# Kernel optimization log

Measured on AMD Instinct MI355X. Metric: run time of the kernel, lower is better.

## Reference

```python
import jax, jax.numpy as jnp
import numpy as np

B = 32          # graphs in batch
NP = 1000       # nodes per graph (uniform -> static TopK)
N = B * NP      # total nodes
DEG = 10
E = N * DEG     # intra-graph edges
H, D = 4, 128   # heads, per-head dim (GATConv(32,128,heads=4))
F_IN = 32
HD = H * D      # 512
K = int(np.ceil(0.8 * NP))  # TopKPooling ratio=0.8 -> 800 kept per graph
SLOPE = 0.2     # GATConv leaky_relu negative slope


def setup_inputs() -> dict:
    key = jax.random.key(0)
    ks = jax.random.split(key, 16)
    x = jax.random.normal(ks[0], (N, F_IN), jnp.float32)
    off = (jnp.arange(B, dtype=jnp.int64) * NP)[:, None]
    src = (jax.random.randint(ks[1], (B, NP * DEG), 0, NP) + off).reshape(-1)
    dst = (jax.random.randint(ks[2], (B, NP * DEG), 0, NP) + off).reshape(-1)
    edge_index = jnp.stack([src, dst]).astype(jnp.int64)
    batch = jnp.repeat(jnp.arange(B, dtype=jnp.int64), NP)
    edge_attr = jax.random.normal(ks[3], (E, 16), jnp.float32)
    # GATConv params
    W = jax.random.normal(ks[4], (F_IN, HD), jnp.float32) / np.sqrt(F_IN)
    att_src = jax.random.normal(ks[5], (H, D), jnp.float32) * 0.1
    att_dst = jax.random.normal(ks[6], (H, D), jnp.float32) * 0.1
    bias = jnp.zeros((HD,), jnp.float32)
    # TopKPooling weight
    topk_w = jax.random.normal(ks[7], (HD,), jnp.float32)
    # MLP head
    lin1_w = jax.random.normal(ks[8], (2 * HD, 128), jnp.float32) / np.sqrt(2 * HD)
    lin1_b = jnp.zeros((128,), jnp.float32)
    lin2_w = jax.random.normal(ks[9], (128, 64), jnp.float32) / np.sqrt(128)
    lin2_b = jnp.zeros((64,), jnp.float32)
    lin3_w = jax.random.normal(ks[10], (64, 8), jnp.float32) / np.sqrt(64)
    lin3_b = jnp.zeros((8,), jnp.float32)
    return dict(x=x, edge_index=edge_index, batch=batch, edge_attr=edge_attr,
                W=W, att_src=att_src, att_dst=att_dst, bias=bias, topk_w=topk_w,
                lin1_w=lin1_w, lin1_b=lin1_b, lin2_w=lin2_w, lin2_b=lin2_b,
                lin3_w=lin3_w, lin3_b=lin3_b)


def reference(x, edge_index, batch, edge_attr, W, att_src, att_dst, bias, topk_w,
              lin1_w, lin1_b, lin2_w, lin2_b, lin3_w, lin3_b):
    # ---- GATConv(32,128,heads=4), concat, default self-loops ----
    loop = jnp.arange(N, dtype=edge_index.dtype)
    src = jnp.concatenate([edge_index[0], loop])
    dst = jnp.concatenate([edge_index[1], loop])
    h = (x @ W).reshape(N, H, D)                       # [N,H,D]
    a_s = jnp.einsum('nhd,hd->nh', h, att_src)         # [N,H]
    a_d = jnp.einsum('nhd,hd->nh', h, att_dst)
    e = jax.nn.leaky_relu(a_s[src] + a_d[dst], SLOPE)  # [E2,H]
    m = jax.ops.segment_max(e, dst, num_segments=N)    # per-dst softmax (stable)
    ex = jnp.exp(e - m[dst])
    denom = jax.ops.segment_sum(ex, dst, num_segments=N)
    alpha = ex / denom[dst]                            # [E2,H]
    agg = jax.ops.segment_sum(alpha[:, :, None] * h[src], dst, num_segments=N)
    x1 = jax.nn.relu(agg.reshape(N, HD) + bias)        # [N,512]
    # ---- TopKPooling(512, ratio=0.8), tanh nonlinearity ----
    score = jnp.tanh((x1 @ topk_w) / jnp.linalg.norm(topk_w))  # [N]
    vals, idx = jax.lax.top_k(score.reshape(B, NP), K)         # [B,K]
    xg = x1.reshape(B, NP, HD)
    xs = jnp.take_along_axis(xg, idx[:, :, None], axis=1) * vals[:, :, None]
    # ---- global max + mean pool, MLP head (eval: dropout = identity) ----
    x2 = jnp.concatenate([xs.max(axis=1), xs.mean(axis=1)], axis=-1)  # [B,1024]
    h1 = jax.nn.relu(x2 @ lin1_w + lin1_b)
    h2 = jax.nn.relu(h1 @ lin2_w + lin2_b)
    return jax.nn.log_softmax(h2 @ lin3_w + lin3_b, axis=-1)  # [B,8]
```

## Files before the change

kernel.cpp:

```cpp
#include <hip/hip_runtime.h>
#include <hip/hip_fp16.h>
#include <math.h>


#define N_NODES 32000
#define B_GRAPHS 32
#define NPG 1000
#define DEGC 10
#define E_EDGES (N_NODES*DEGC)
#define HD 512
#define F_IN 32
#define KKEEP 800
#define SLOPE 0.2f
#define CAP 32

__global__ void prep_kernel(const float* __restrict__ W, const float* __restrict__ att_src,
                            const float* __restrict__ att_dst, const float* __restrict__ topk_w,
                            float* __restrict__ Ws, float* __restrict__ Wd, float* __restrict__ misc,
                            int* __restrict__ counts)
{
    int tid = threadIdx.x;
    if (blockIdx.x > 0) {
        int i = (blockIdx.x - 1)*256 + tid;
        if (i < N_NODES/4) ((int4*)counts)[i] = make_int4(0,0,0,0);
        return;
    }
    if (tid < 128) {
        int f = tid >> 2, hh = tid & 3;
        float s1 = 0.f, s2 = 0.f;
        for (int d = 0; d < 128; ++d) {
            float w = W[f*HD + hh*128 + d];
            s1 = fmaf(w, att_src[hh*128 + d], s1);
            s2 = fmaf(w, att_dst[hh*128 + d], s2);
        }
        Ws[f*4+hh] = s1;
        Wd[f*4+hh] = s2;
    }
    __shared__ float red[256];
    float tw0 = topk_w[tid], tw1 = topk_w[tid+256];
    red[tid] = tw0*tw0 + tw1*tw1;
    __syncthreads();
    for (int s = 128; s > 0; s >>= 1) { if (tid < s) red[tid] += red[tid+s]; __syncthreads(); }
    if (tid == 0) misc[0] = 1.0f / sqrtf(red[0]);
}

#define NPB 32
#define CH_BLOCKS 1000
#define BS_BLOCKS 128
__global__ __launch_bounds__(256) void stage1_kernel(
    const float* __restrict__ x, const float* __restrict__ W,
    const float* __restrict__ Ws, const float* __restrict__ Wd,
    const int* __restrict__ dst,
    __half* __restrict__ h, float* __restrict__ a_s, float* __restrict__ a_d,
    int* __restrict__ counts, int* __restrict__ slots)
{
    int b = blockIdx.x;
    int tid = threadIdx.x;
    if (b < CH_BLOCKS) {
        __shared__ float s_x[NPB*F_IN];
        int n0 = (b & 7)*4000 + (b >> 3)*NPB;
        float wc0[F_IN], wc1[F_IN];
        #pragma unroll
        for (int f = 0; f < F_IN; ++f) {
            float2 wp = *(const float2*)(W + f*HD + 2*tid);
            wc0[f] = wp.x;
            wc1[f] = wp.y;
        }
        const float4* xg = (const float4*)(x + (size_t)n0*F_IN);
        float4* sx4 = (float4*)s_x;
        if (tid < NPB*F_IN/4) sx4[tid] = xg[tid];
        __syncthreads();
        for (int n = 0; n < NPB; ++n) {
            const float4* xr = (const float4*)(s_x + n*F_IN);
            float acc0 = 0.f, acc1 = 0.f;
            #pragma unroll
            for (int f4 = 0; f4 < F_IN/4; ++f4) {
                float4 xv = xr[f4];
                acc0 = fmaf(xv.x, wc0[f4*4+0], acc0); acc1 = fmaf(xv.x, wc1[f4*4+0], acc1);
                acc0 = fmaf(xv.y, wc0[f4*4+1], acc0); acc1 = fmaf(xv.y, wc1[f4*4+1], acc1);
                acc0 = fmaf(xv.z, wc0[f4*4+2], acc0); acc1 = fmaf(xv.z, wc1[f4*4+2], acc1);
                acc0 = fmaf(xv.w, wc0[f4*4+3], acc0); acc1 = fmaf(xv.w, wc1[f4*4+3], acc1);
            }
            *(__half2*)(h + (size_t)(n0+n)*HD + 2*tid) = __floats2half2_rn(acc0, acc1);
        }
        {
            int n = tid >> 3, hh = (tid >> 1) & 3, which = tid & 1;
            const float* Wx = which ? Wd : Ws;
            const float* xr = s_x + n*F_IN;
            float s = 0.f;
            #pragma unroll
            for (int f = 0; f < F_IN; ++f) s = fmaf(xr[f], Wx[f*4+hh], s);
            float* dp = which ? a_d : a_s;
            dp[(size_t)(n0+n)*4 + hh] = s;
        }
    } else {
        int i = (b - CH_BLOCKS)*256 + tid;
        int stride = BS_BLOCKS*256;
        for (; i < E_EDGES; i += stride) {
            int d = dst[i];
            int p = atomicAdd(&counts[d], 1);
            if (p < CAP) slots[d*CAP + p] = i;
        }
    }
}

__global__ __launch_bounds__(256) void gat_agg_kernel(
    const __half* __restrict__ h, const float* __restrict__ a_s, const float* __restrict__ a_d,
    const int* __restrict__ counts, const int* __restrict__ slots, const int* __restrict__ esrc,
    const float* __restrict__ bias, const float* __restrict__ topk_w, const float* __restrict__ misc,
    __half* __restrict__ x1, float* __restrict__ scores)
{
    __shared__ int    s_src[4][CAP];
    __shared__ float4 s_al4[4][CAP];
    int tid = threadIdx.x;
    int wid = tid >> 6, lane = tid & 63;
    int grp  = (blockIdx.x & 7) * 1000 + (blockIdx.x >> 3);
    int node = grp*4 + wid;
    int deg  = min(counts[node], CAP);

    int key = (lane < deg) ? slots[node*CAP + lane] : (0x7FFF0000 + lane);
    int rank = 0;
    for (int j = 0; j < deg; ++j) rank += (__shfl(key, j, 64) < key);
    if (lane >= deg) rank = lane;
    int sorted_eid = __builtin_amdgcn_ds_permute(rank << 2, key);

    int src = node;
    if (lane < deg) src = esrc[sorted_eid];

    float4 ad    = *(const float4*)(a_d + (size_t)node*4);
    float4 aself = *(const float4*)(a_s + (size_t)node*4);
    float4 asrc  = make_float4(0.f,0.f,0.f,0.f);
    if (lane < deg) asrc = *(const float4*)(a_s + (size_t)src*4);

    float ex[4], exs[4];
    {
        float u;
        u = asrc.x + ad.x;  ex[0]  = u > 0.f ? u : SLOPE*u;
        u = asrc.y + ad.y;  ex[1]  = u > 0.f ? u : SLOPE*u;
        u = asrc.z + ad.z;  ex[2]  = u > 0.f ? u : SLOPE*u;
        u = asrc.w + ad.w;  ex[3]  = u > 0.f ? u : SLOPE*u;
        u = aself.x + ad.x; exs[0] = __expf(u > 0.f ? u : SLOPE*u);
        u = aself.y + ad.y; exs[1] = __expf(u > 0.f ? u : SLOPE*u);
        u = aself.z + ad.z; exs[2] = __expf(u > 0.f ? u : SLOPE*u);
        u = aself.w + ad.w; exs[3] = __expf(u > 0.f ? u : SLOPE*u);
    }
    float al[4], alself[4];
    #pragma unroll
    for (int hh = 0; hh < 4; ++hh) {
        float e = (lane < deg) ? __expf(ex[hh]) : 0.f;
        float den = e;
        #pragma unroll
        for (int msk = 1; msk < 64; msk <<= 1) den += __shfl_xor(den, msk, 64);
        den += exs[hh];
        float inv = __builtin_amdgcn_rcpf(den);
        al[hh]     = e * inv;
        alself[hh] = exs[hh] * inv;
    }
    if (lane < deg) {
        s_src[wid][lane] = src;
        s_al4[wid][lane] = make_float4(al[0], al[1], al[2], al[3]);
    }
    __syncthreads();

    int head = lane >> 4;
    const __half* hb = h + lane*8;
    const float* alw = (const float*)&s_al4[wid][0];
    float f0=0.f,f1=0.f,f2=0.f,f3=0.f,f4=0.f,f5=0.f,f6=0.f,f7=0.f;
    #define MIX_LO(ACC,A,Q) asm("v_fma_mix_f32 %0, %1, %2, %0 op_sel_hi:[0,1,0]" : "+v"(ACC) : "v"(A), "v"(Q))
    #define MIX_HI(ACC,A,Q) asm("v_fma_mix_f32 %0, %1, %2, %0 op_sel:[0,1,0] op_sel_hi:[0,1,0]" : "+v"(ACC) : "v"(A), "v"(Q))
    #define EDGE_STEP(E_IDX)                                                          \
        {   int se = s_src[wid][E_IDX];                                               \
            float av = alw[(E_IDX)*4 + head];                                         \
            uint4 q = *(const uint4*)(hb + (size_t)se*HD);                            \
            MIX_LO(f0, av, q.x); MIX_HI(f1, av, q.x);                                 \
            MIX_LO(f2, av, q.y); MIX_HI(f3, av, q.y);                                 \
            MIX_LO(f4, av, q.z); MIX_HI(f5, av, q.z);                                 \
            MIX_LO(f6, av, q.w); MIX_HI(f7, av, q.w); }
    int e = 0;
    for (; e + 2 <= deg; e += 2) { EDGE_STEP(e); EDGE_STEP(e+1); }
    if (e < deg) EDGE_STEP(e);
    #undef EDGE_STEP
    {
        float a01 = (head & 1) ? alself[1] : alself[0];
        float a23 = (head & 1) ? alself[3] : alself[2];
        float av  = (head & 2) ? a23 : a01;
        uint4 q = *(const uint4*)(hb + (size_t)node*HD);
        MIX_LO(f0, av, q.x); MIX_HI(f1, av, q.x);
        MIX_LO(f2, av, q.y); MIX_HI(f3, av, q.y);
        MIX_LO(f4, av, q.z); MIX_HI(f5, av, q.z);
        MIX_LO(f6, av, q.w); MIX_HI(f7, av, q.w);
    }
    #undef MIX_LO
    #undef MIX_HI

    int c0 = lane*8;
    float4 b0 = *(const float4*)(bias + c0);
    float4 b1 = *(const float4*)(bias + c0 + 4);
    float v0 = fmaxf(f0 + b0.x, 0.f), v1 = fmaxf(f1 + b0.y, 0.f);
    float v2 = fmaxf(f2 + b0.z, 0.f), v3 = fmaxf(f3 + b0.w, 0.f);
    float v4 = fmaxf(f4 + b1.x, 0.f), v5 = fmaxf(f5 + b1.y, 0.f);
    float v6 = fmaxf(f6 + b1.z, 0.f), v7 = fmaxf(f7 + b1.w, 0.f);
    {
        __half2 p0 = __floats2half2_rn(v0, v1);
        __half2 p1 = __floats2half2_rn(v2, v3);
        __half2 p2 = __floats2half2_rn(v4, v5);
        __half2 p3 = __floats2half2_rn(v6, v7);
        uint4 pk;
        pk.x = *(unsigned*)&p0; pk.y = *(unsigned*)&p1;
        pk.z = *(unsigned*)&p2; pk.w = *(unsigned*)&p3;
        *(uint4*)(x1 + (size_t)node*HD + c0) = pk;
    }

    float4 tw0 = *(const float4*)(topk_w + c0);
    float4 tw1 = *(const float4*)(topk_w + c0 + 4);
    float p = v0*tw0.x + v1*tw0.y + v2*tw0.z + v3*tw0.w
            + v4*tw1.x + v5*tw1.y + v6*tw1.z + v7*tw1.w;
    #pragma unroll
    for (int msk = 1; msk < 64; msk <<= 1) p += __shfl_xor(p, msk, 64);
    if (lane == 0) {
        float dotv = p * misc[0];
        float eu   = __expf(2.f * fabsf(dotv));
        float th   = 1.f - 2.f/(eu + 1.f);
        scores[node] = copysignf(th, dotv);
    }
}

__global__ __launch_bounds__(256) void topk_kernel(const float* __restrict__ scores,
                                                   int* __restrict__ kept_ids,
                                                   float* __restrict__ kept_vals)
{
    int g = blockIdx.x, part = blockIdx.y;
    __shared__ float s[NPG];
    int tid = threadIdx.x;
    for (int i = tid; i < NPG; i += 256) s[i] = scores[g*NPG + i];
    __syncthreads();
    int i = part*250 + tid;
    if (tid < 250) {
        float si = s[i];
        int rank = 0;
        for (int j = 0; j < NPG; ++j) {
            float sj = s[j];
            rank += (sj > si) || (sj == si && j < i);
        }
        if (rank < KKEEP) {
            kept_ids[g*KKEEP + rank]  = g*NPG + i;
            kept_vals[g*KKEEP + rank] = si;
        }
    }
}

#define RCHUNK 50
#define NCHUNK 16
__global__ __launch_bounds__(128) void pool_partial_kernel(
    const __half* __restrict__ x1, const int* __restrict__ kept_ids,
    const float* __restrict__ kept_vals, float* __restrict__ pmax, float* __restrict__ psum)
{
    int bid = blockIdx.x;
    int k = bid & 7, q = bid >> 3;
    int g = k*4 + (q & 3), c = q >> 2;
    int tid = threadIdx.x;
    __shared__ int   ids[RCHUNK];
    __shared__ float vals[RCHUNK];
    if (tid < RCHUNK) {
        ids[tid]  = kept_ids[g*KKEEP + c*RCHUNK + tid];
        vals[tid] = kept_vals[g*KKEEP + c*RCHUNK + tid];
    }
    __syncthreads();
    float4 mxA = make_float4(-INFINITY,-INFINITY,-INFINITY,-INFINITY), mxB = mxA;
    float4 smA = make_float4(0.f,0.f,0.f,0.f), smB = smA;
    for (int r = 0; r < RCHUNK; r += 2) {
        const __half2* pA = (const __half2*)(x1 + (size_t)ids[r]*HD + tid*4);
        const __half2* pB = (const __half2*)(x1 + (size_t)ids[r+1]*HD + tid*4);
        __half2 qA0 = pA[0], qA1 = pA[1], qB0 = pB[0], qB1 = pB[1];
        float2 a0 = __half22float2(qA0), a1 = __half22float2(qA1);
        float2 b0 = __half22float2(qB0), b1 = __half22float2(qB1);
        float lA = vals[r], lB = vals[r+1];
        float4 vA = make_float4(a0.x*lA, a0.y*lA, a1.x*lA, a1.y*lA);
        float4 vB = make_float4(b0.x*lB, b0.y*lB, b1.x*lB, b1.y*lB);
        mxA.x = fmaxf(mxA.x, vA.x); mxA.y = fmaxf(mxA.y, vA.y);
        mxA.z = fmaxf(mxA.z, vA.z); mxA.w = fmaxf(mxA.w, vA.w);
        mxB.x = fmaxf(mxB.x, vB.x); mxB.y = fmaxf(mxB.y, vB.y);
        mxB.z = fmaxf(mxB.z, vB.z); mxB.w = fmaxf(mxB.w, vB.w);
        smA.x += vA.x; smA.y += vA.y; smA.z += vA.z; smA.w += vA.w;
        smB.x += vB.x; smB.y += vB.y; smB.z += vB.z; smB.w += vB.w;
    }
    float4 mx, sm;
    mx.x = fmaxf(mxA.x, mxB.x); mx.y = fmaxf(mxA.y, mxB.y);
    mx.z = fmaxf(mxA.z, mxB.z); mx.w = fmaxf(mxA.w, mxB.w);
    sm.x = smA.x + smB.x; sm.y = smA.y + smB.y;
    sm.z = smA.z + smB.z; sm.w = smA.w + smB.w;
    *(float4*)(pmax + (size_t)(g*NCHUNK + c)*HD + tid*4) = mx;
    *(float4*)(psum + (size_t)(g*NCHUNK + c)*HD + tid*4) = sm;
}

__global__ __launch_bounds__(256) void mlp_kernel(
    const float* __restrict__ pmax, const float* __restrict__ psum,
    const float* __restrict__ w1, const float* __restrict__ b1,
    const float* __restrict__ w2, const float* __restrict__ b2,
    const float* __restrict__ w3, const float* __restrict__ b3,
    float* __restrict__ out)
{
    int g = blockIdx.x;
    int tid = threadIdx.x;
    __shared__ float sx[1024];
    __shared__ float part1[8][128];
    __shared__ float sh1[128];
    __shared__ float part2[4][64];
    __shared__ float sh2[64];
    __shared__ float part3[8][8];
    __shared__ float slog[8];

    {
        int half = tid >> 7;
        int c4 = tid & 127;
        const float* basep = half ? psum : pmax;
        float4 r = *(const float4*)(basep + (size_t)(g*NCHUNK)*HD + c4*4);
        #pragma unroll
        for (int c = 1; c < NCHUNK; ++c) {
            float4 v = *(const float4*)(basep + (size_t)(g*NCHUNK + c)*HD + c4*4);
            if (half) { r.x += v.x; r.y += v.y; r.z += v.z; r.w += v.w; }
            else {
                r.x = fmaxf(r.x, v.x); r.y = fmaxf(r.y, v.y);
                r.z = fmaxf(r.z, v.z); r.w = fmaxf(r.w, v.w);
            }
        }
        if (half) { const float inv = 1.0f/KKEEP; r.x *= inv; r.y *= inv; r.z *= inv; r.w *= inv; }
        *(float4*)(sx + half*512 + c4*4) = r;
    }
    __syncthreads();

    {
        int ks = tid >> 5, tc = tid & 31;
        const float* w1p = w1 + (size_t)(ks*128)*128 + tc*4;
        const float* sxp = sx + ks*128;
        float4 acc = make_float4(0.f,0.f,0.f,0.f);
        #pragma unroll 8
        for (int k = 0; k < 128; ++k) {
            float xk = sxp[k];
            float4 w = *(const float4*)(w1p + (size_t)k*128);
            acc.x = fmaf(xk, w.x, acc.x); acc.y = fmaf(xk, w.y, acc.y);
            acc.z = fmaf(xk, w.z, acc.z); acc.w = fmaf(xk, w.w, acc.w);
        }
        *(float4*)(&part1[ks][tc*4]) = acc;
    }
    __syncthreads();
    if (tid < 128) {
        float s = b1[tid];
        #pragma unroll
        for (int p = 0; p < 8; ++p) s += part1[p][tid];
        sh1[tid] = fmaxf(s, 0.0f);
    }
    __syncthreads();

    {
        int ks2 = tid >> 6, to = tid & 63;
        float a = 0.f;
        #pragma unroll 8
        for (int k = 0; k < 32; ++k) {
            int kk = ks2*32 + k;
            a = fmaf(sh1[kk], w2[kk*64 + to], a);
        }
        part2[ks2][to] = a;
    }
    __syncthreads();
    if (tid < 64) {
        float s = b2[tid];
        #pragma unroll
        for (int p = 0; p < 4; ++p) s += part2[p][tid];
        sh2[tid] = fmaxf(s, 0.0f);
    }
    __syncthreads();

    if (tid < 64) {
        int ks3 = tid >> 3, o = tid & 7;
        float a = 0.f;
        #pragma unroll
        for (int k = 0; k < 8; ++k) {
            int kk = ks3*8 + k;
            a = fmaf(sh2[kk], w3[kk*8 + o], a);
        }
        part3[ks3][o] = a;
    }
    __syncthreads();
    if (tid < 8) {
        float s = b3[tid];
        #pragma unroll
        for (int p = 0; p < 8; ++p) s += part3[p][tid];
        slog[tid] = s;
    }
    __syncthreads();
    if (tid == 0) {
        float m = slog[0];
        for (int i = 1; i < 8; ++i) m = fmaxf(m, slog[i]);
        float ssum = 0.0f;
        for (int i = 0; i < 8; ++i) ssum += expf(slog[i] - m);
        float lse = m + logf(ssum);
        for (int i = 0; i < 8; ++i) out[g*8 + i] = slog[i] - lse;
    }
}

extern "C" void kernel_launch(void* const* d_in, const int* in_sizes, int n_in,
                              void* d_out, int out_size, void* d_ws, size_t ws_size,
                              hipStream_t stream) {
    const float* x        = (const float*)d_in[0];
    const int*   ei       = (const int*)d_in[1];
    const float* W        = (const float*)d_in[4];
    const float* att_src  = (const float*)d_in[5];
    const float* att_dst  = (const float*)d_in[6];
    const float* bias     = (const float*)d_in[7];
    const float* topk_w   = (const float*)d_in[8];
    const float* w1       = (const float*)d_in[9];
    const float* b1       = (const float*)d_in[10];
    const float* w2       = (const float*)d_in[11];
    const float* b2       = (const float*)d_in[12];
    const float* w3       = (const float*)d_in[13];
    const float* b3       = (const float*)d_in[14];
    float* out = (float*)d_out;

    const int* src = ei;
    const int* dst = ei + E_EDGES;

    char* wsb = (char*)d_ws;
    size_t off = 0;
    auto alloc = [&](size_t bytes) -> void* {
        void* p = (void*)(wsb + off);
        off += (bytes + 255) & ~(size_t)255;
        return p;
    };
    __half* h       = (__half*)alloc((size_t)N_NODES*HD*2);
    __half* x1      = (__half*)alloc((size_t)N_NODES*HD*2);
    float* a_s      = (float*)alloc((size_t)N_NODES*4*4);
    float* a_d      = (float*)alloc((size_t)N_NODES*4*4);
    float* Ws       = (float*)alloc(F_IN*4*4);
    float* Wd       = (float*)alloc(F_IN*4*4);
    float* misc     = (float*)alloc(256);
    int*   counts   = (int*)alloc((size_t)N_NODES*4);
    int*   slots    = (int*)alloc((size_t)N_NODES*CAP*4);
    float* scores   = (float*)alloc((size_t)N_NODES*4);
    int*   kept_ids = (int*)alloc((size_t)B_GRAPHS*KKEEP*4);
    float* kept_vals= (float*)alloc((size_t)B_GRAPHS*KKEEP*4);
    float* pmax     = (float*)alloc((size_t)B_GRAPHS*NCHUNK*HD*4);
    float* psum     = (float*)alloc((size_t)B_GRAPHS*NCHUNK*HD*4);

    prep_kernel<<<33, 256, 0, stream>>>(W, att_src, att_dst, topk_w, Ws, Wd, misc, counts);
    stage1_kernel<<<CH_BLOCKS + BS_BLOCKS, 256, 0, stream>>>(
        x, W, Ws, Wd, dst, h, a_s, a_d, counts, slots);
    gat_agg_kernel<<<N_NODES/4, 256, 0, stream>>>(h, a_s, a_d, counts, slots, src,
                                                  bias, topk_w, misc, x1, scores);
    topk_kernel<<<dim3(B_GRAPHS, 4), 256, 0, stream>>>(scores, kept_ids, kept_vals);
    pool_partial_kernel<<<B_GRAPHS*NCHUNK, 128, 0, stream>>>(x1, kept_ids, kept_vals, pmax, psum);
    mlp_kernel<<<B_GRAPHS, 256, 0, stream>>>(pmax, psum, w1, b1, w2, b2, w3, b3, out);
}
```

Baseline: 119.3 us.

## Fuse top-k selection, pooling and MLP head into one per-graph tail kernel

Replaces the separate top-k ranking, partial pooling and MLP kernels with a single kernel per graph. Top-k ranks go to shared memory and the kept rows are pooled directly, with no global intermediates for kept ids or partial max/sum. This removes two launches and the global round-trips, but the tail now runs on only 32 blocks, so the gather-heavy pooling has far less parallelism and memory-level concurrency.

```diff
diff --git a/kernel.cpp b/kernel.cpp
--- a/kernel.cpp
+++ b/kernel.cpp
@@ -225,76 +225,8 @@
     }
 }
 
-__global__ __launch_bounds__(256) void topk_kernel(const float* __restrict__ scores,
-                                                   int* __restrict__ kept_ids,
-                                                   float* __restrict__ kept_vals)
-{
-    int g = blockIdx.x, part = blockIdx.y;
-    __shared__ float s[NPG];
-    int tid = threadIdx.x;
-    for (int i = tid; i < NPG; i += 256) s[i] = scores[g*NPG + i];
-    __syncthreads();
-    int i = part*250 + tid;
-    if (tid < 250) {
-        float si = s[i];
-        int rank = 0;
-        for (int j = 0; j < NPG; ++j) {
-            float sj = s[j];
-            rank += (sj > si) || (sj == si && j < i);
-        }
-        if (rank < KKEEP) {
-            kept_ids[g*KKEEP + rank]  = g*NPG + i;
-            kept_vals[g*KKEEP + rank] = si;
-        }
-    }
-}
-
-#define RCHUNK 50
-#define NCHUNK 16
-__global__ __launch_bounds__(128) void pool_partial_kernel(
-    const __half* __restrict__ x1, const int* __restrict__ kept_ids,
-    const float* __restrict__ kept_vals, float* __restrict__ pmax, float* __restrict__ psum)
-{
-    int bid = blockIdx.x;
-    int k = bid & 7, q = bid >> 3;
-    int g = k*4 + (q & 3), c = q >> 2;
-    int tid = threadIdx.x;
-    __shared__ int   ids[RCHUNK];
-    __shared__ float vals[RCHUNK];
-    if (tid < RCHUNK) {
-        ids[tid]  = kept_ids[g*KKEEP + c*RCHUNK + tid];
-        vals[tid] = kept_vals[g*KKEEP + c*RCHUNK + tid];
-    }
-    __syncthreads();
-    float4 mxA = make_float4(-INFINITY,-INFINITY,-INFINITY,-INFINITY), mxB = mxA;
-    float4 smA = make_float4(0.f,0.f,0.f,0.f), smB = smA;
-    for (int r = 0; r < RCHUNK; r += 2) {
-        const __half2* pA = (const __half2*)(x1 + (size_t)ids[r]*HD + tid*4);
-        const __half2* pB = (const __half2*)(x1 + (size_t)ids[r+1]*HD + tid*4);
-        __half2 qA0 = pA[0], qA1 = pA[1], qB0 = pB[0], qB1 = pB[1];
-        float2 a0 = __half22float2(qA0), a1 = __half22float2(qA1);
-        float2 b0 = __half22float2(qB0), b1 = __half22float2(qB1);
-        float lA = vals[r], lB = vals[r+1];
-        float4 vA = make_float4(a0.x*lA, a0.y*lA, a1.x*lA, a1.y*lA);
-        float4 vB = make_float4(b0.x*lB, b0.y*lB, b1.x*lB, b1.y*lB);
-        mxA.x = fmaxf(mxA.x, vA.x); mxA.y = fmaxf(mxA.y, vA.y);
-        mxA.z = fmaxf(mxA.z, vA.z); mxA.w = fmaxf(mxA.w, vA.w);
-        mxB.x = fmaxf(mxB.x, vB.x); mxB.y = fmaxf(mxB.y, vB.y);
-        mxB.z = fmaxf(mxB.z, vB.z); mxB.w = fmaxf(mxB.w, vB.w);
-        smA.x += vA.x; smA.y += vA.y; smA.z += vA.z; smA.w += vA.w;
-        smB.x += vB.x; smB.y += vB.y; smB.z += vB.z; smB.w += vB.w;
-    }
-    float4 mx, sm;
-    mx.x = fmaxf(mxA.x, mxB.x); mx.y = fmaxf(mxA.y, mxB.y);
-    mx.z = fmaxf(mxA.z, mxB.z); mx.w = fmaxf(mxA.w, mxB.w);
-    sm.x = smA.x + smB.x; sm.y = smA.y + smB.y;
-    sm.z = smA.z + smB.z; sm.w = smA.w + smB.w;
-    *(float4*)(pmax + (size_t)(g*NCHUNK + c)*HD + tid*4) = mx;
-    *(float4*)(psum + (size_t)(g*NCHUNK + c)*HD + tid*4) = sm;
-}
-
-__global__ __launch_bounds__(256) void mlp_kernel(
-    const float* __restrict__ pmax, const float* __restrict__ psum,
+__global__ __launch_bounds__(512) void tail_kernel(
+    const float* __restrict__ scores, const __half* __restrict__ x1,
     const float* __restrict__ w1, const float* __restrict__ b1,
     const float* __restrict__ w2, const float* __restrict__ b2,
     const float* __restrict__ w3, const float* __restrict__ b3,
@@ -302,40 +234,67 @@
 {
     int g = blockIdx.x;
     int tid = threadIdx.x;
+    __shared__ float s[NPG];
+    __shared__ int   kid[KKEEP];
+    __shared__ float kval[KKEEP];
+    __shared__ float pm[2][512];
+    __shared__ float ps[2][512];
     __shared__ float sx[1024];
-    __shared__ float part1[8][128];
+    __shared__ float part1[16][128];
     __shared__ float sh1[128];
-    __shared__ float part2[4][64];
+    __shared__ float part2[8][64];
     __shared__ float sh2[64];
     __shared__ float part3[8][8];
     __shared__ float slog[8];
 
-    {
-        int half = tid >> 7;
-        int c4 = tid & 127;
-        const float* basep = half ? psum : pmax;
-        float4 r = *(const float4*)(basep + (size_t)(g*NCHUNK)*HD + c4*4);
-        #pragma unroll
-        for (int c = 1; c < NCHUNK; ++c) {
-            float4 v = *(const float4*)(basep + (size_t)(g*NCHUNK + c)*HD + c4*4);
-            if (half) { r.x += v.x; r.y += v.y; r.z += v.z; r.w += v.w; }
-            else {
-                r.x = fmaxf(r.x, v.x); r.y = fmaxf(r.y, v.y);
-                r.z = fmaxf(r.z, v.z); r.w = fmaxf(r.w, v.w);
-            }
-        }
-        if (half) { const float inv = 1.0f/KKEEP; r.x *= inv; r.y *= inv; r.z *= inv; r.w *= inv; }
-        *(float4*)(sx + half*512 + c4*4) = r;
+    for (int i = tid; i < NPG; i += 512) s[i] = scores[g*NPG + i];
+    __syncthreads();
+    for (int i = tid; i < NPG; i += 512) {
+        float si = s[i];
+        int rank = 0;
+        for (int j = 0; j < NPG; ++j) {
+            float sj = s[j];
+            rank += (sj > si) || (sj == si && j < i);
+        }
+        if (rank < KKEEP) { kid[rank] = i; kval[rank] = si; }
+    }
+    __syncthreads();
+
+    {
+        int c2 = (tid & 255) * 2;
+        int rh = tid >> 8;
+        float2 mx = make_float2(-INFINITY, -INFINITY);
+        float2 sm = make_float2(0.f, 0.f);
+        int r0 = rh * 400;
+        #pragma unroll 4
+        for (int r = r0; r < r0 + 400; ++r) {
+            __half2 q = *(const __half2*)(x1 + (size_t)(g*NPG + kid[r])*HD + c2);
+            float2 f = __half22float2(q);
+            float kv = kval[r];
+            f.x *= kv; f.y *= kv;
+            mx.x = fmaxf(mx.x, f.x); mx.y = fmaxf(mx.y, f.y);
+            sm.x += f.x;             sm.y += f.y;
+        }
+        pm[rh][c2] = mx.x; pm[rh][c2+1] = mx.y;
+        ps[rh][c2] = sm.x; ps[rh][c2+1] = sm.y;
+    }
+    __syncthreads();
+    {
+        int col = tid;
+        if (col < 512) {
+            sx[col]       = fmaxf(pm[0][col], pm[1][col]);
+            sx[512 + col] = (ps[0][col] + ps[1][col]) * (1.0f/KKEEP);
+        }
     }
     __syncthreads();
 
     {
         int ks = tid >> 5, tc = tid & 31;
-        const float* w1p = w1 + (size_t)(ks*128)*128 + tc*4;
-        const float* sxp = sx + ks*128;
+        const float* w1p = w1 + (size_t)(ks*64)*128 + tc*4;
+        const float* sxp = sx + ks*64;
         float4 acc = make_float4(0.f,0.f,0.f,0.f);
         #pragma unroll 8
-        for (int k = 0; k < 128; ++k) {
+        for (int k = 0; k < 64; ++k) {
             float xk = sxp[k];
             float4 w = *(const float4*)(w1p + (size_t)k*128);
             acc.x = fmaf(xk, w.x, acc.x); acc.y = fmaf(xk, w.y, acc.y);
@@ -345,29 +304,29 @@
     }
     __syncthreads();
     if (tid < 128) {
-        float s = b1[tid];
-        #pragma unroll
-        for (int p = 0; p < 8; ++p) s += part1[p][tid];
-        sh1[tid] = fmaxf(s, 0.0f);
+        float v = b1[tid];
+        #pragma unroll
+        for (int p = 0; p < 16; ++p) v += part1[p][tid];
+        sh1[tid] = fmaxf(v, 0.0f);
     }
     __syncthreads();
 
     {
         int ks2 = tid >> 6, to = tid & 63;
         float a = 0.f;
-        #pragma unroll 8
-        for (int k = 0; k < 32; ++k) {
-            int kk = ks2*32 + k;
+        #pragma unroll
+        for (int k = 0; k < 16; ++k) {
+            int kk = ks2*16 + k;
             a = fmaf(sh1[kk], w2[kk*64 + to], a);
         }
         part2[ks2][to] = a;
     }
     __syncthreads();
     if (tid < 64) {
-        float s = b2[tid];
-        #pragma unroll
-        for (int p = 0; p < 4; ++p) s += part2[p][tid];
-        sh2[tid] = fmaxf(s, 0.0f);
+        float v = b2[tid];
+        #pragma unroll
+        for (int p = 0; p < 8; ++p) v += part2[p][tid];
+        sh2[tid] = fmaxf(v, 0.0f);
     }
     __syncthreads();
 
@@ -383,10 +342,10 @@
     }
     __syncthreads();
     if (tid < 8) {
-        float s = b3[tid];
-        #pragma unroll
-        for (int p = 0; p < 8; ++p) s += part3[p][tid];
-        slog[tid] = s;
+        float v = b3[tid];
+        #pragma unroll
+        for (int p = 0; p < 8; ++p) v += part3[p][tid];
+        slog[tid] = v;
     }
     __syncthreads();
     if (tid == 0) {
@@ -437,17 +396,11 @@
     int*   counts   = (int*)alloc((size_t)N_NODES*4);
     int*   slots    = (int*)alloc((size_t)N_NODES*CAP*4);
     float* scores   = (float*)alloc((size_t)N_NODES*4);
-    int*   kept_ids = (int*)alloc((size_t)B_GRAPHS*KKEEP*4);
-    float* kept_vals= (float*)alloc((size_t)B_GRAPHS*KKEEP*4);
-    float* pmax     = (float*)alloc((size_t)B_GRAPHS*NCHUNK*HD*4);
-    float* psum     = (float*)alloc((size_t)B_GRAPHS*NCHUNK*HD*4);
 
     prep_kernel<<<33, 256, 0, stream>>>(W, att_src, att_dst, topk_w, Ws, Wd, misc, counts);
     stage1_kernel<<<CH_BLOCKS + BS_BLOCKS, 256, 0, stream>>>(
         x, W, Ws, Wd, dst, h, a_s, a_d, counts, slots);
     gat_agg_kernel<<<N_NODES/4, 256, 0, stream>>>(h, a_s, a_d, counts, slots, src,
                                                   bias, topk_w, misc, x1, scores);
-    topk_kernel<<<dim3(B_GRAPHS, 4), 256, 0, stream>>>(scores, kept_ids, kept_vals);
-    pool_partial_kernel<<<B_GRAPHS*NCHUNK, 128, 0, stream>>>(x1, kept_ids, kept_vals, pmax, psum);
-    mlp_kernel<<<B_GRAPHS, 256, 0, stream>>>(pmax, psum, w1, b1, w2, b2, w3, b3, out);
+    tail_kernel<<<B_GRAPHS, 512, 0, stream>>>(scores, x1, w1, b1, w2, b2, w3, b3, out);
 }
```

After: 170.4 us. 42.8% more time.

## Fuse top-k selection with pooling and drop edge sorting in GAT aggregation

Applied to the files above, without the earlier changes.

Merges the top-k ranking and the max/mean pooling into one kernel. Each block ranks its 250 rows and then streams those rows contiguously, masking out the ones that are not kept, so the kept-id and kept-value arrays and one launch go away. In the aggregation kernel, the per-node sort of edge slots is removed and edges are used in their atomic-insertion order. This makes fp32 summation order nondeterministic. The edge loop is also unrolled by four so more gathers are in flight. The pooling now reads all rows, not only the kept ones, and the mlp_kernel must handle NCHUNK=4 partials instead of 16.

```diff
diff --git a/kernel.cpp b/kernel.cpp
--- a/kernel.cpp
+++ b/kernel.cpp
@@ -118,14 +118,8 @@
     int node = grp*4 + wid;
     int deg  = min(counts[node], CAP);
 
-    int key = (lane < deg) ? slots[node*CAP + lane] : (0x7FFF0000 + lane);
-    int rank = 0;
-    for (int j = 0; j < deg; ++j) rank += (__shfl(key, j, 64) < key);
-    if (lane >= deg) rank = lane;
-    int sorted_eid = __builtin_amdgcn_ds_permute(rank << 2, key);
-
     int src = node;
-    if (lane < deg) src = esrc[sorted_eid];
+    if (lane < deg) src = esrc[slots[node*CAP + lane]];
 
     float4 ad    = *(const float4*)(a_d + (size_t)node*4);
     float4 aself = *(const float4*)(a_s + (size_t)node*4);
@@ -168,28 +162,37 @@
     float f0=0.f,f1=0.f,f2=0.f,f3=0.f,f4=0.f,f5=0.f,f6=0.f,f7=0.f;
     #define MIX_LO(ACC,A,Q) asm("v_fma_mix_f32 %0, %1, %2, %0 op_sel_hi:[0,1,0]" : "+v"(ACC) : "v"(A), "v"(Q))
     #define MIX_HI(ACC,A,Q) asm("v_fma_mix_f32 %0, %1, %2, %0 op_sel:[0,1,0] op_sel_hi:[0,1,0]" : "+v"(ACC) : "v"(A), "v"(Q))
-    #define EDGE_STEP(E_IDX)                                                          \
-        {   int se = s_src[wid][E_IDX];                                               \
-            float av = alw[(E_IDX)*4 + head];                                         \
-            uint4 q = *(const uint4*)(hb + (size_t)se*HD);                            \
-            MIX_LO(f0, av, q.x); MIX_HI(f1, av, q.x);                                 \
-            MIX_LO(f2, av, q.y); MIX_HI(f3, av, q.y);                                 \
-            MIX_LO(f4, av, q.z); MIX_HI(f5, av, q.z);                                 \
-            MIX_LO(f6, av, q.w); MIX_HI(f7, av, q.w); }
+    #define MIX8(AV,Q) { \
+        MIX_LO(f0, AV, Q.x); MIX_HI(f1, AV, Q.x); \
+        MIX_LO(f2, AV, Q.y); MIX_HI(f3, AV, Q.y); \
+        MIX_LO(f4, AV, Q.z); MIX_HI(f5, AV, Q.z); \
+        MIX_LO(f6, AV, Q.w); MIX_HI(f7, AV, Q.w); }
     int e = 0;
-    for (; e + 2 <= deg; e += 2) { EDGE_STEP(e); EDGE_STEP(e+1); }
-    if (e < deg) EDGE_STEP(e);
-    #undef EDGE_STEP
+    for (; e + 4 <= deg; e += 4) {
+        int se0 = s_src[wid][e],   se1 = s_src[wid][e+1];
+        int se2 = s_src[wid][e+2], se3 = s_src[wid][e+3];
+        float av0 = alw[(e+0)*4 + head], av1 = alw[(e+1)*4 + head];
+        float av2 = alw[(e+2)*4 + head], av3 = alw[(e+3)*4 + head];
+        uint4 q0 = *(const uint4*)(hb + (size_t)se0*HD);
+        uint4 q1 = *(const uint4*)(hb + (size_t)se1*HD);
+        uint4 q2 = *(const uint4*)(hb + (size_t)se2*HD);
+        uint4 q3 = *(const uint4*)(hb + (size_t)se3*HD);
+        MIX8(av0, q0) MIX8(av1, q1) MIX8(av2, q2) MIX8(av3, q3)
+    }
+    for (; e < deg; ++e) {
+        int se = s_src[wid][e];
+        float av = alw[e*4 + head];
+        uint4 q = *(const uint4*)(hb + (size_t)se*HD);
+        MIX8(av, q)
+    }
     {
         float a01 = (head & 1) ? alself[1] : alself[0];
         float a23 = (head & 1) ? alself[3] : alself[2];
         float av  = (head & 2) ? a23 : a01;
         uint4 q = *(const uint4*)(hb + (size_t)node*HD);
-        MIX_LO(f0, av, q.x); MIX_HI(f1, av, q.x);
-        MIX_LO(f2, av, q.y); MIX_HI(f3, av, q.y);
-        MIX_LO(f4, av, q.z); MIX_HI(f5, av, q.z);
-        MIX_LO(f6, av, q.w); MIX_HI(f7, av, q.w);
-    }
+        MIX8(av, q)
+    }
+    #undef MIX8
     #undef MIX_LO
     #undef MIX_HI
 
@@ -225,72 +228,57 @@
     }
 }
 
-__global__ __launch_bounds__(256) void topk_kernel(const float* __restrict__ scores,
-                                                   int* __restrict__ kept_ids,
-                                                   float* __restrict__ kept_vals)
+#define PROWS 250
+#define NCHUNK 4
+__global__ __launch_bounds__(256) void topk_pool_kernel(
+    const float* __restrict__ scores, const __half* __restrict__ x1,
+    float* __restrict__ pmax, float* __restrict__ psum)
 {
-    int g = blockIdx.x, part = blockIdx.y;
+    int bid = blockIdx.x;
+    int k = bid & 7, q = bid >> 3;
+    int g = k*4 + (q & 3), part = q >> 2;
+    int tid = threadIdx.x;
     __shared__ float s[NPG];
-    int tid = threadIdx.x;
+    __shared__ float kv[PROWS];
+    __shared__ int   kf[PROWS];
     for (int i = tid; i < NPG; i += 256) s[i] = scores[g*NPG + i];
     __syncthreads();
-    int i = part*250 + tid;
-    if (tid < 250) {
+    if (tid < PROWS) {
+        int i = part*PROWS + tid;
         float si = s[i];
         int rank = 0;
         for (int j = 0; j < NPG; ++j) {
             float sj = s[j];
             rank += (sj > si) || (sj == si && j < i);
         }
-        if (rank < KKEEP) {
-            kept_ids[g*KKEEP + rank]  = g*NPG + i;
-            kept_vals[g*KKEEP + rank] = si;
-        }
-    }
-}
-
-#define RCHUNK 50
-#define NCHUNK 16
-__global__ __launch_bounds__(128) void pool_partial_kernel(
-    const __half* __restrict__ x1, const int* __restrict__ kept_ids,
-    const float* __restrict__ kept_vals, float* __restrict__ pmax, float* __restrict__ psum)
-{
-    int bid = blockIdx.x;
-    int k = bid & 7, q = bid >> 3;
-    int g = k*4 + (q & 3), c = q >> 2;
-    int tid = threadIdx.x;
-    __shared__ int   ids[RCHUNK];
-    __shared__ float vals[RCHUNK];
-    if (tid < RCHUNK) {
-        ids[tid]  = kept_ids[g*KKEEP + c*RCHUNK + tid];
-        vals[tid] = kept_vals[g*KKEEP + c*RCHUNK + tid];
-    }
-    __syncthreads();
-    float4 mxA = make_float4(-INFINITY,-INFINITY,-INFINITY,-INFINITY), mxB = mxA;
-    float4 smA = make_float4(0.f,0.f,0.f,0.f), smB = smA;
-    for (int r = 0; r < RCHUNK; r += 2) {
-        const __half2* pA = (const __half2*)(x1 + (size_t)ids[r]*HD + tid*4);
-        const __half2* pB = (const __half2*)(x1 + (size_t)ids[r+1]*HD + tid*4);
-        __half2 qA0 = pA[0], qA1 = pA[1], qB0 = pB[0], qB1 = pB[1];
-        float2 a0 = __half22float2(qA0), a1 = __half22float2(qA1);
-        float2 b0 = __half22float2(qB0), b1 = __half22float2(qB1);
-        float lA = vals[r], lB = vals[r+1];
-        float4 vA = make_float4(a0.x*lA, a0.y*lA, a1.x*lA, a1.y*lA);
-        float4 vB = make_float4(b0.x*lB, b0.y*lB, b1.x*lB, b1.y*lB);
-        mxA.x = fmaxf(mxA.x, vA.x); mxA.y = fmaxf(mxA.y, vA.y);
-        mxA.z = fmaxf(mxA.z, vA.z); mxA.w = fmaxf(mxA.w, vA.w);
-        mxB.x = fmaxf(mxB.x, vB.x); mxB.y = fmaxf(mxB.y, vB.y);
-        mxB.z = fmaxf(mxB.z, vB.z); mxB.w = fmaxf(mxB.w, vB.w);
-        smA.x += vA.x; smA.y += vA.y; smA.z += vA.z; smA.w += vA.w;
-        smB.x += vB.x; smB.y += vB.y; smB.z += vB.z; smB.w += vB.w;
-    }
-    float4 mx, sm;
-    mx.x = fmaxf(mxA.x, mxB.x); mx.y = fmaxf(mxA.y, mxB.y);
-    mx.z = fmaxf(mxA.z, mxB.z); mx.w = fmaxf(mxA.w, mxB.w);
-    sm.x = smA.x + smB.x; sm.y = smA.y + smB.y;
-    sm.z = smA.z + smB.z; sm.w = smA.w + smB.w;
-    *(float4*)(pmax + (size_t)(g*NCHUNK + c)*HD + tid*4) = mx;
-    *(float4*)(psum + (size_t)(g*NCHUNK + c)*HD + tid*4) = sm;
+        kf[tid] = (rank < KKEEP);
+        kv[tid] = si;
+    }
+    __syncthreads();
+    int c2 = tid*2;
+    const __half* xb = x1 + (size_t)(g*NPG + part*PROWS)*HD + c2;
+    float2 mx = make_float2(-INFINITY, -INFINITY);
+    float2 sm = make_float2(0.f, 0.f);
+    for (int r = 0; r < PROWS; r += 2) {
+        __half2 hA = *(const __half2*)(xb + (size_t)r*HD);
+        __half2 hB = *(const __half2*)(xb + (size_t)(r+1)*HD);
+        if (kf[r]) {
+            float2 f = __half22float2(hA);
+            float v = kv[r];
+            f.x *= v; f.y *= v;
+            mx.x = fmaxf(mx.x, f.x); mx.y = fmaxf(mx.y, f.y);
+            sm.x += f.x;             sm.y += f.y;
+        }
+        if (kf[r+1]) {
+            float2 f = __half22float2(hB);
+            float v = kv[r+1];
+            f.x *= v; f.y *= v;
+            mx.x = fmaxf(mx.x, f.x); mx.y = fmaxf(mx.y, f.y);
+            sm.x += f.x;             sm.y += f.y;
+        }
+    }
+    *(float2*)(pmax + (size_t)(g*NCHUNK + part)*HD + c2) = mx;
+    *(float2*)(psum + (size_t)(g*NCHUNK + part)*HD + c2) = sm;
 }
 
 __global__ __launch_bounds__(256) void mlp_kernel(
@@ -437,8 +425,6 @@
     int*   counts   = (int*)alloc((size_t)N_NODES*4);
     int*   slots    = (int*)alloc((size_t)N_NODES*CAP*4);
     float* scores   = (float*)alloc((size_t)N_NODES*4);
-    int*   kept_ids = (int*)alloc((size_t)B_GRAPHS*KKEEP*4);
-    float* kept_vals= (float*)alloc((size_t)B_GRAPHS*KKEEP*4);
     float* pmax     = (float*)alloc((size_t)B_GRAPHS*NCHUNK*HD*4);
     float* psum     = (float*)alloc((size_t)B_GRAPHS*NCHUNK*HD*4);
 
@@ -447,7 +433,6 @@
         x, W, Ws, Wd, dst, h, a_s, a_d, counts, slots);
     gat_agg_kernel<<<N_NODES/4, 256, 0, stream>>>(h, a_s, a_d, counts, slots, src,
                                                   bias, topk_w, misc, x1, scores);
-    topk_kernel<<<dim3(B_GRAPHS, 4), 256, 0, stream>>>(scores, kept_ids, kept_vals);
-    pool_partial_kernel<<<B_GRAPHS*NCHUNK, 128, 0, stream>>>(x1, kept_ids, kept_vals, pmax, psum);
+    topk_pool_kernel<<<B_GRAPHS*NCHUNK, 256, 0, stream>>>(scores, x1, pmax, psum);
     mlp_kernel<<<B_GRAPHS, 256, 0, stream>>>(pmax, psum, w1, b1, w2, b2, w3, b3, out);
 }
```

Measured after the change: 148.2 us. 1.24x slower.

## Drop per-node edge sort and unroll gather loop by four

Applied to the files above, without the earlier changes.

Removes the in-wave ranking sort of edge slots, which put incoming edges into a deterministic order, and reads edge ids directly in slot order. The aggregation loop is unrolled by four so four neighbour row loads are in flight before the FMA chains run. The aim is to cut the O(deg) shuffle loop and raise memory-level parallelism. Slot order comes from atomics, so summation order, and with it floating-point rounding, can now vary between runs.

```diff
diff --git a/kernel.cpp b/kernel.cpp
--- a/kernel.cpp
+++ b/kernel.cpp
@@ -118,14 +118,8 @@
     int node = grp*4 + wid;
     int deg  = min(counts[node], CAP);
 
-    int key = (lane < deg) ? slots[node*CAP + lane] : (0x7FFF0000 + lane);
-    int rank = 0;
-    for (int j = 0; j < deg; ++j) rank += (__shfl(key, j, 64) < key);
-    if (lane >= deg) rank = lane;
-    int sorted_eid = __builtin_amdgcn_ds_permute(rank << 2, key);
-
     int src = node;
-    if (lane < deg) src = esrc[sorted_eid];
+    if (lane < deg) src = esrc[slots[node*CAP + lane]];
 
     float4 ad    = *(const float4*)(a_d + (size_t)node*4);
     float4 aself = *(const float4*)(a_s + (size_t)node*4);
@@ -168,28 +162,37 @@
     float f0=0.f,f1=0.f,f2=0.f,f3=0.f,f4=0.f,f5=0.f,f6=0.f,f7=0.f;
     #define MIX_LO(ACC,A,Q) asm("v_fma_mix_f32 %0, %1, %2, %0 op_sel_hi:[0,1,0]" : "+v"(ACC) : "v"(A), "v"(Q))
     #define MIX_HI(ACC,A,Q) asm("v_fma_mix_f32 %0, %1, %2, %0 op_sel:[0,1,0] op_sel_hi:[0,1,0]" : "+v"(ACC) : "v"(A), "v"(Q))
-    #define EDGE_STEP(E_IDX)                                                          \
-        {   int se = s_src[wid][E_IDX];                                               \
-            float av = alw[(E_IDX)*4 + head];                                         \
-            uint4 q = *(const uint4*)(hb + (size_t)se*HD);                            \
-            MIX_LO(f0, av, q.x); MIX_HI(f1, av, q.x);                                 \
-            MIX_LO(f2, av, q.y); MIX_HI(f3, av, q.y);                                 \
-            MIX_LO(f4, av, q.z); MIX_HI(f5, av, q.z);                                 \
-            MIX_LO(f6, av, q.w); MIX_HI(f7, av, q.w); }
+    #define MIX8(AV,Q) { \
+        MIX_LO(f0, AV, Q.x); MIX_HI(f1, AV, Q.x); \
+        MIX_LO(f2, AV, Q.y); MIX_HI(f3, AV, Q.y); \
+        MIX_LO(f4, AV, Q.z); MIX_HI(f5, AV, Q.z); \
+        MIX_LO(f6, AV, Q.w); MIX_HI(f7, AV, Q.w); }
     int e = 0;
-    for (; e + 2 <= deg; e += 2) { EDGE_STEP(e); EDGE_STEP(e+1); }
-    if (e < deg) EDGE_STEP(e);
-    #undef EDGE_STEP
+    for (; e + 4 <= deg; e += 4) {
+        int se0 = s_src[wid][e],   se1 = s_src[wid][e+1];
+        int se2 = s_src[wid][e+2], se3 = s_src[wid][e+3];
+        float av0 = alw[(e+0)*4 + head], av1 = alw[(e+1)*4 + head];
+        float av2 = alw[(e+2)*4 + head], av3 = alw[(e+3)*4 + head];
+        uint4 q0 = *(const uint4*)(hb + (size_t)se0*HD);
+        uint4 q1 = *(const uint4*)(hb + (size_t)se1*HD);
+        uint4 q2 = *(const uint4*)(hb + (size_t)se2*HD);
+        uint4 q3 = *(const uint4*)(hb + (size_t)se3*HD);
+        MIX8(av0, q0) MIX8(av1, q1) MIX8(av2, q2) MIX8(av3, q3)
+    }
+    for (; e < deg; ++e) {
+        int se = s_src[wid][e];
+        float av = alw[e*4 + head];
+        uint4 q = *(const uint4*)(hb + (size_t)se*HD);
+        MIX8(av, q)
+    }
     {
         float a01 = (head & 1) ? alself[1] : alself[0];
         float a23 = (head & 1) ? alself[3] : alself[2];
         float av  = (head & 2) ? a23 : a01;
         uint4 q = *(const uint4*)(hb + (size_t)node*HD);
-        MIX_LO(f0, av, q.x); MIX_HI(f1, av, q.x);
-        MIX_LO(f2, av, q.y); MIX_HI(f3, av, q.y);
-        MIX_LO(f4, av, q.z); MIX_HI(f5, av, q.z);
-        MIX_LO(f6, av, q.w); MIX_HI(f7, av, q.w);
-    }
+        MIX8(av, q)
+    }
+    #undef MIX8
     #undef MIX_LO
     #undef MIX_HI
 
```

Measured after the change: 117.5 us, median of 2. About the same (-1.6%).
